# Optimization experiments

Measured on AMD Instinct MI355X. Metric: run time of the kernel, lower is better.

The kernel has to match this reference:

```python
import jax, jax.numpy as jnp
import numpy as np

# config[4]: SparseConv3d(32, 64, k=3, stride=2, pad=1) on a (21,800,704) voxel grid, nnz=220939
IN_DIMS = (21, 800, 704)   # (x, y, z) spatial extents
KSIZE   = (3, 3, 3)
STRIDE  = (2, 2, 2)
PAD     = (1, 1, 1)
CIN, COUT = 32, 64
NNZ = 220939
OUT_DIMS = tuple((IN_DIMS[d] + 2 * PAD[d] - KSIZE[d]) // STRIDE[d] + 1 for d in range(3))  # (11,400,352)


def setup_inputs() -> dict:
    key = jax.random.key(0)
    k1, k2, k3 = jax.random.split(key, 3)
    features = jax.random.normal(k1, (NNZ, CIN), dtype=jnp.float32)
    coords = jnp.stack(
        [jax.random.randint(jax.random.fold_in(k2, d), (NNZ,), 0, IN_DIMS[d]) for d in range(3)],
        axis=1,
    ).astype(jnp.int32)
    # spconv weight layout: one [Cin, Cout] GEMM per kernel offset (27 offsets)
    weight = jax.random.normal(k3, (KSIZE[0] * KSIZE[1] * KSIZE[2], CIN, COUT), dtype=jnp.float32) * 0.05
    return {"features": features, "coords": coords, "weight": weight}


def reference(features, coords, weight):
    # Rulebook gather-GEMM-scatter, vectorized over points; static loop over 27 offsets.
    # out[o] += W[k] @ in[i] where i = o*stride - pad + k, i.e. o = (coord_i + pad - k)/stride.
    n_out = OUT_DIMS[0] * OUT_DIMS[1] * OUT_DIMS[2]
    stride = jnp.array(STRIDE, jnp.int32)
    pad = jnp.array(PAD, jnp.int32)
    odims = jnp.array(OUT_DIMS, jnp.int32)
    out = jnp.zeros((n_out + 1, COUT), features.dtype)  # last row = dump slot for invalid
    kidx = 0
    for kx in range(KSIZE[0]):
        for ky in range(KSIZE[1]):
            for kz in range(KSIZE[2]):
                off = jnp.array([kx, ky, kz], jnp.int32)
                o = coords + pad - off                      # [N,3]
                oq = o // stride
                valid = jnp.all((o >= 0) & (o % stride == 0) & (oq < odims), axis=1)
                flat = (oq[:, 0] * OUT_DIMS[1] + oq[:, 1]) * OUT_DIMS[2] + oq[:, 2]
                flat = jnp.where(valid, flat, n_out)
                contrib = features @ weight[kidx]           # [N, Cout] per-offset GEMM
                out = out.at[flat].add(contrib)             # scatter-accumulate
                kidx += 1
    # Densified sparse-conv output (inactive output sites are exactly zero)
    return out[:-1].reshape(OUT_DIMS + (COUT,))
```

## Files before the change

### kernel.cpp

```cpp
#include <hip/hip_runtime.h>


#define CIN  32
#define COUT 64
#define OXD  11
#define OYD  400
#define OZD  352

constexpr int CHUNKS = 96;

typedef float v2f __attribute__((ext_vector_type(2)));

__global__ __launch_bounds__(256) void zero_out_k(float4* __restrict__ out4,
                                                  int n4, int* __restrict__ gcnt) {
    const int i = blockIdx.x * 256 + threadIdx.x;
    if (i < n4) out4[i] = make_float4(0.f, 0.f, 0.f, 0.f);
    if (i < 27) gcnt[i] = 0;
}

__global__ __launch_bounds__(256) void build_pairs(
    const int* __restrict__ coords, int2* __restrict__ arena,
    int* __restrict__ gcnt, int nnz)
{
    __shared__ int lcnt[27];
    __shared__ int lbase[27];
    const int t = threadIdx.x;
    if (t < 27) lcnt[t] = 0;
    __syncthreads();

    const int n = blockIdx.x * 256 + t;
    int ncomb = 0;
    int ck[8], cls[8], csite[8];
    if (n < nnz) {
        const int cx = coords[3 * n + 0];
        const int cy = coords[3 * n + 1];
        const int cz = coords[3 * n + 2];
        int kxl[2], oxl[2], nx;
        int kyl[2], oyl[2], ny;
        int kzl[2], ozl[2], nz;
        {
            const int c1 = cx + 1;
            if (c1 & 1) { kxl[0] = 1; oxl[0] = c1 >> 1; nx = 1; }
            else { kxl[0] = 2; oxl[0] = (c1 - 2) >> 1; nx = 1;
                   if ((c1 >> 1) < OXD) { kxl[1] = 0; oxl[1] = c1 >> 1; nx = 2; } }
        }
        {
            const int c1 = cy + 1;
            if (c1 & 1) { kyl[0] = 1; oyl[0] = c1 >> 1; ny = 1; }
            else { kyl[0] = 2; oyl[0] = (c1 - 2) >> 1; ny = 1;
                   if ((c1 >> 1) < OYD) { kyl[1] = 0; oyl[1] = c1 >> 1; ny = 2; } }
        }
        {
            const int c1 = cz + 1;
            if (c1 & 1) { kzl[0] = 1; ozl[0] = c1 >> 1; nz = 1; }
            else { kzl[0] = 2; ozl[0] = (c1 - 2) >> 1; nz = 1;
                   if ((c1 >> 1) < OZD) { kzl[1] = 0; ozl[1] = c1 >> 1; nz = 2; } }
        }
        for (int ix = 0; ix < nx; ++ix)
            for (int iy = 0; iy < ny; ++iy)
                for (int iz = 0; iz < nz; ++iz) {
                    const int k = kxl[ix] * 9 + kyl[iy] * 3 + kzl[iz];
                    const int site = (oxl[ix] * OYD + oyl[iy]) * OZD + ozl[iz];
                    ck[ncomb] = k;
                    csite[ncomb] = site;
                    cls[ncomb] = atomicAdd(&lcnt[k], 1);
                    ++ncomb;
                }
    }
    __syncthreads();
    if (t < 27) lbase[t] = atomicAdd(&gcnt[t], lcnt[t]);
    __syncthreads();
    for (int c = 0; c < ncomb; ++c) {
        const int k = ck[c];
        arena[(size_t)k * nnz + lbase[k] + cls[c]] = make_int2(n, csite[c]);
    }
}

__global__ __launch_bounds__(256) void spconv_scatter(
    const float* __restrict__ feat,
    const float* __restrict__ weight,
    const int2*  __restrict__ arena,
    const int*   __restrict__ gcnt,
    float*       __restrict__ out,
    int nnz)
{
    __shared__ float lds[4][8][64][4];

    const int lane = threadIdx.x & 63;
    const int wid  = threadIdx.x >> 6;
    const int k     = blockIdx.x % 27;
    const int chunk = blockIdx.x / 27;
    const int cnt = gcnt[k];
    if (cnt == 0) return;

    v2f w2[16];
    const float* __restrict__ Wk = weight + (size_t)k * CIN * COUT;
    #pragma unroll
    for (int i = 0; i < 16; ++i) {
        w2[i][0] = Wk[(2 * i + 0) * COUT + lane];
        w2[i][1] = Wk[(2 * i + 1) * COUT + lane];
    }

    const int NW = CHUNKS * 4;
    const int widk = chunk * 4 + wid;
    const int C = (cnt + NW - 1) / NW;
    const int start = widk * C;
    const int end   = min(start + C, cnt);
    const int2* __restrict__ ak = arena + (size_t)k * nnz;
    float* __restrict__ outl = out + lane;

    for (int i0 = start; i0 < end; i0 += 64) {
        const int take = min(64, end - i0);
        const int idx = min(i0 + lane, end - 1);
        const int2 pr = ak[idx];

        const float4* __restrict__ fr4 = (const float4*)(feat + (size_t)pr.x * CIN);
        float4 r[8];
        #pragma unroll
        for (int b = 0; b < 8; ++b) r[b] = fr4[b];
        #pragma unroll
        for (int b = 0; b < 8; ++b) *(float4*)&lds[wid][b][lane][0] = r[b];
        asm volatile("s_waitcnt lgkmcnt(0)" ::: "memory");

        for (int j = 0; j < take; ++j) {
            v2f a0 = {0.f, 0.f}, a1 = {0.f, 0.f};
            #pragma unroll
            for (int b = 0; b < 8; ++b) {
                const float4 f = *(const float4*)&lds[wid][b][j][0];
                v2f f01 = {f.x, f.y};
                v2f f23 = {f.z, f.w};
#if __has_builtin(__builtin_elementwise_fma)
                a0 = __builtin_elementwise_fma(f01, w2[2 * b + 0], a0);
                a1 = __builtin_elementwise_fma(f23, w2[2 * b + 1], a1);
#else
                a0[0] = fmaf(f01[0], w2[2 * b + 0][0], a0[0]);
                a0[1] = fmaf(f01[1], w2[2 * b + 0][1], a0[1]);
                a1[0] = fmaf(f23[0], w2[2 * b + 1][0], a1[0]);
                a1[1] = fmaf(f23[1], w2[2 * b + 1][1], a1[1]);
#endif
            }
            const int st = __builtin_amdgcn_readlane(pr.y, j);
            const float acc = (a0[0] + a0[1]) + (a1[0] + a1[1]);
            atomicAdd(outl + (size_t)st * COUT, acc);
        }
    }
}

extern "C" void kernel_launch(void* const* d_in, const int* in_sizes, int n_in,
                              void* d_out, int out_size, void* d_ws, size_t ws_size,
                              hipStream_t stream) {
    const float* feat   = (const float*)d_in[0];
    const int*   coords = (const int*)d_in[1];
    const float* weight = (const float*)d_in[2];
    float*       out    = (float*)d_out;
    const int nnz = in_sizes[0] / CIN;

    int2* arena = (int2*)d_ws;
    int*  gcnt  = (int*)(arena + (size_t)27 * nnz);

    const int n4 = out_size / 4;
    zero_out_k<<<(n4 + 255) / 256, 256, 0, stream>>>((float4*)out, n4, gcnt);
    build_pairs<<<(nnz + 255) / 256, 256, 0, stream>>>(coords, arena, gcnt, nnz);
    spconv_scatter<<<27 * CHUNKS, 256, 0, stream>>>(feat, weight, arena, gcnt, out, nnz);
}
```

Measured before the change: 570.4 us.

## Bucket pairs by output tile and accumulate in LDS, removing global zero-fill

Rebuilds the rulebook as per-output-tile buckets of 128 sites, each with a fixed capacity and a global overflow list. One block per bucket sorts its pairs by kernel offset, accumulates contributions with LDS atomics into a 128x64 tile, then writes the whole tile out. This removes the separate global zero pass and replaces global float atomics with coalesced stores. In exchange, features are read directly from global memory per pair, per-thread transposed weights are reloaded whenever the offset changes, and the whole output must be covered by buckets. An overflow path handles buckets that exceed capacity, but anything beyond the overflow cap is silently dropped.

```diff
diff --git a/kernel.cpp b/kernel.cpp
--- a/kernel.cpp
+++ b/kernel.cpp
@@ -1,148 +1,212 @@
 #include <hip/hip_runtime.h>
 
 
-#define CIN  32
-#define COUT 64
-#define OXD  11
-#define OYD  400
-#define OZD  352
-
-constexpr int CHUNKS = 96;
+#define CIN    32
+#define COUT   64
+#define OXD    11
+#define OYD    400
+#define OZD    352
+#define NOUT   (OXD * OYD * OZD)
+#define BSITES 128
+#define NBUCK  (NOUT / BSITES)
+#define CAP    256
+#define OVCAP  32768
+#define NWT    (27 * COUT * CIN)
 
 typedef float v2f __attribute__((ext_vector_type(2)));
 
-__global__ __launch_bounds__(256) void zero_out_k(float4* __restrict__ out4,
-                                                  int n4, int* __restrict__ gcnt) {
+__global__ __launch_bounds__(256) void prep(const float* __restrict__ w,
+                                            float* __restrict__ wt,
+                                            int* __restrict__ gcnt,
+                                            int* __restrict__ ovcnt) {
     const int i = blockIdx.x * 256 + threadIdx.x;
-    if (i < n4) out4[i] = make_float4(0.f, 0.f, 0.f, 0.f);
-    if (i < 27) gcnt[i] = 0;
+    if (i < NWT) {
+        const int k  = i >> 11;
+        const int rm = i & 2047;
+        const int co = rm >> 5;
+        const int ci = rm & 31;
+        wt[i] = w[k * (CIN * COUT) + ci * COUT + co];
+    }
+    if (i < NBUCK) gcnt[i] = 0;
+    if (i == NBUCK) *ovcnt = 0;
 }
 
 __global__ __launch_bounds__(256) void build_pairs(
-    const int* __restrict__ coords, int2* __restrict__ arena,
-    int* __restrict__ gcnt, int nnz)
-{
-    __shared__ int lcnt[27];
-    __shared__ int lbase[27];
-    const int t = threadIdx.x;
-    if (t < 27) lcnt[t] = 0;
-    __syncthreads();
-
-    const int n = blockIdx.x * 256 + t;
-    int ncomb = 0;
-    int ck[8], cls[8], csite[8];
-    if (n < nnz) {
-        const int cx = coords[3 * n + 0];
-        const int cy = coords[3 * n + 1];
-        const int cz = coords[3 * n + 2];
-        int kxl[2], oxl[2], nx;
-        int kyl[2], oyl[2], ny;
-        int kzl[2], ozl[2], nz;
-        {
-            const int c1 = cx + 1;
-            if (c1 & 1) { kxl[0] = 1; oxl[0] = c1 >> 1; nx = 1; }
-            else { kxl[0] = 2; oxl[0] = (c1 - 2) >> 1; nx = 1;
-                   if ((c1 >> 1) < OXD) { kxl[1] = 0; oxl[1] = c1 >> 1; nx = 2; } }
-        }
-        {
-            const int c1 = cy + 1;
-            if (c1 & 1) { kyl[0] = 1; oyl[0] = c1 >> 1; ny = 1; }
-            else { kyl[0] = 2; oyl[0] = (c1 - 2) >> 1; ny = 1;
-                   if ((c1 >> 1) < OYD) { kyl[1] = 0; oyl[1] = c1 >> 1; ny = 2; } }
-        }
-        {
-            const int c1 = cz + 1;
-            if (c1 & 1) { kzl[0] = 1; ozl[0] = c1 >> 1; nz = 1; }
-            else { kzl[0] = 2; ozl[0] = (c1 - 2) >> 1; nz = 1;
-                   if ((c1 >> 1) < OZD) { kzl[1] = 0; ozl[1] = c1 >> 1; nz = 2; } }
-        }
-        for (int ix = 0; ix < nx; ++ix)
-            for (int iy = 0; iy < ny; ++iy)
-                for (int iz = 0; iz < nz; ++iz) {
-                    const int k = kxl[ix] * 9 + kyl[iy] * 3 + kzl[iz];
-                    const int site = (oxl[ix] * OYD + oyl[iy]) * OZD + ozl[iz];
-                    ck[ncomb] = k;
-                    csite[ncomb] = site;
-                    cls[ncomb] = atomicAdd(&lcnt[k], 1);
-                    ++ncomb;
-                }
-    }
-    __syncthreads();
-    if (t < 27) lbase[t] = atomicAdd(&gcnt[t], lcnt[t]);
-    __syncthreads();
-    for (int c = 0; c < ncomb; ++c) {
-        const int k = ck[c];
-        arena[(size_t)k * nnz + lbase[k] + cls[c]] = make_int2(n, csite[c]);
-    }
-}
-
-__global__ __launch_bounds__(256) void spconv_scatter(
-    const float* __restrict__ feat,
-    const float* __restrict__ weight,
-    const int2*  __restrict__ arena,
-    const int*   __restrict__ gcnt,
-    float*       __restrict__ out,
+    const int* __restrict__ coords,
+    int* __restrict__ arena,
+    int* __restrict__ gcnt,
+    int* __restrict__ ovcnt,
+    int2* __restrict__ ovlist,
     int nnz)
 {
-    __shared__ float lds[4][8][64][4];
-
+    const int n = blockIdx.x * 256 + threadIdx.x;
+    if (n >= nnz) return;
+
+    const int cx = coords[3 * n + 0];
+    const int cy = coords[3 * n + 1];
+    const int cz = coords[3 * n + 2];
+
+    int kxl[2], oxl[2], nx;
+    int kyl[2], oyl[2], ny;
+    int kzl[2], ozl[2], nz;
+    {
+        const int c1 = cx + 1;
+        if (c1 & 1) { kxl[0] = 1; oxl[0] = c1 >> 1; nx = 1; }
+        else { kxl[0] = 2; oxl[0] = (c1 - 2) >> 1; nx = 1;
+               if ((c1 >> 1) < OXD) { kxl[1] = 0; oxl[1] = c1 >> 1; nx = 2; } }
+    }
+    {
+        const int c1 = cy + 1;
+        if (c1 & 1) { kyl[0] = 1; oyl[0] = c1 >> 1; ny = 1; }
+        else { kyl[0] = 2; oyl[0] = (c1 - 2) >> 1; ny = 1;
+               if ((c1 >> 1) < OYD) { kyl[1] = 0; oyl[1] = c1 >> 1; ny = 2; } }
+    }
+    {
+        const int c1 = cz + 1;
+        if (c1 & 1) { kzl[0] = 1; ozl[0] = c1 >> 1; nz = 1; }
+        else { kzl[0] = 2; ozl[0] = (c1 - 2) >> 1; nz = 1;
+               if ((c1 >> 1) < OZD) { kzl[1] = 0; ozl[1] = c1 >> 1; nz = 2; } }
+    }
+
+    for (int ix = 0; ix < nx; ++ix)
+        for (int iy = 0; iy < ny; ++iy)
+            for (int iz = 0; iz < nz; ++iz) {
+                const int k    = kxl[ix] * 9 + kyl[iy] * 3 + kzl[iz];
+                const int site = (oxl[ix] * OYD + oyl[iy]) * OZD + ozl[iz];
+                const int bkt  = site >> 7;
+                const int loc  = site & (BSITES - 1);
+                const int slot = atomicAdd(&gcnt[bkt], 1);
+                if (slot < CAP) {
+                    arena[(size_t)bkt * CAP + slot] = (n << 12) | (k << 7) | loc;
+                } else {
+                    const int o = atomicAdd(ovcnt, 1);
+                    if (o < OVCAP) ovlist[o] = make_int2(site, (n << 5) | k);
+                }
+            }
+}
+
+__global__ __launch_bounds__(256, 4) void spconv_scatter(
+    const float* __restrict__ feat,
+    const float* __restrict__ wt,
+    const int*   __restrict__ arena,
+    const int*   __restrict__ gcnt,
+    float*       __restrict__ out)
+{
+    __shared__ float tile[BSITES][COUT];
+    __shared__ int   sorted[CAP];
+    __shared__ int   khist[27];
+    __shared__ int   kbase[27];
+
+    const int t    = threadIdx.x;
+    const int lane = t & 63;
+    const int wid  = t >> 6;
+    const int b    = blockIdx.x;
+    const int cnt  = min(gcnt[b], CAP);
+
+    if (t < 27) khist[t] = 0;
+    __syncthreads();
+
+    int myp = 0, myk = 0;
+    if (t < cnt) {
+        myp = arena[(size_t)b * CAP + t];
+        myk = (myp >> 7) & 31;
+        atomicAdd(&khist[myk], 1);
+    }
+    float4* t4 = (float4*)&tile[0][0];
+    #pragma unroll
+    for (int r = 0; r < 8; ++r) t4[t + r * 256] = make_float4(0.f, 0.f, 0.f, 0.f);
+    __syncthreads();
+
+    if (wid == 0) {
+        const int h = (lane < 27) ? khist[lane] : 0;
+        int v = h;
+        #pragma unroll
+        for (int off = 1; off < 32; off <<= 1) {
+            const int u = __shfl_up(v, off);
+            if (lane >= off) v += u;
+        }
+        if (lane < 27) kbase[lane] = v - h;
+    }
+    __syncthreads();
+    if (t < cnt) {
+        const int pos = atomicAdd(&kbase[myk], 1);
+        sorted[pos] = myp;
+    }
+    __syncthreads();
+
+    const int c  = (cnt + 3) >> 2;
+    const int jb = min(wid * c, cnt);
+    const int je = min(jb + c, cnt);
+    float4 wv[8];
+    int curk = -1;
+    for (int j = jb; j < je; ++j) {
+        const int pk  = __builtin_amdgcn_readfirstlane(sorted[j]);
+        const int k   = (pk >> 7) & 31;
+        const int loc = pk & (BSITES - 1);
+        const int pt  = pk >> 12;
+        if (k != curk) {
+            curk = k;
+            const float4* __restrict__ wp =
+                (const float4*)(wt + ((size_t)k * COUT + lane) * CIN);
+            #pragma unroll
+            for (int bb = 0; bb < 8; ++bb) wv[bb] = wp[bb];
+        }
+        const float4* __restrict__ fp = (const float4*)(feat + (size_t)pt * CIN);
+        v2f a0 = {0.f, 0.f}, a1 = {0.f, 0.f};
+        #pragma unroll
+        for (int bb = 0; bb < 8; ++bb) {
+            const float4 f = fp[bb];
+            const float4 wb = wv[bb];
+            v2f f01 = {f.x, f.y}, f23 = {f.z, f.w};
+            v2f w01 = {wb.x, wb.y}, w23 = {wb.z, wb.w};
+#if __has_builtin(__builtin_elementwise_fma)
+            a0 = __builtin_elementwise_fma(f01, w01, a0);
+            a1 = __builtin_elementwise_fma(f23, w23, a1);
+#else
+            a0[0] = fmaf(f01[0], w01[0], a0[0]);
+            a0[1] = fmaf(f01[1], w01[1], a0[1]);
+            a1[0] = fmaf(f23[0], w23[0], a1[0]);
+            a1[1] = fmaf(f23[1], w23[1], a1[1]);
+#endif
+        }
+        atomicAdd(&tile[loc][lane], (a0[0] + a0[1]) + (a1[0] + a1[1]));
+    }
+    __syncthreads();
+
+    float4* __restrict__ o4 = (float4*)(out + (size_t)b * (BSITES * COUT));
+    #pragma unroll
+    for (int r = 0; r < 8; ++r) o4[t + r * 256] = t4[t + r * 256];
+}
+
+__global__ __launch_bounds__(256) void fixup_overflow(
+    const float* __restrict__ feat,
+    const float* __restrict__ wt,
+    const int2*  __restrict__ ovlist,
+    const int*   __restrict__ ovcnt,
+    float*       __restrict__ out)
+{
     const int lane = threadIdx.x & 63;
-    const int wid  = threadIdx.x >> 6;
-    const int k     = blockIdx.x % 27;
-    const int chunk = blockIdx.x / 27;
-    const int cnt = gcnt[k];
-    if (cnt == 0) return;
-
-    v2f w2[16];
-    const float* __restrict__ Wk = weight + (size_t)k * CIN * COUT;
-    #pragma unroll
-    for (int i = 0; i < 16; ++i) {
-        w2[i][0] = Wk[(2 * i + 0) * COUT + lane];
-        w2[i][1] = Wk[(2 * i + 1) * COUT + lane];
-    }
-
-    const int NW = CHUNKS * 4;
-    const int widk = chunk * 4 + wid;
-    const int C = (cnt + NW - 1) / NW;
-    const int start = widk * C;
-    const int end   = min(start + C, cnt);
-    const int2* __restrict__ ak = arena + (size_t)k * nnz;
-    float* __restrict__ outl = out + lane;
-
-    for (int i0 = start; i0 < end; i0 += 64) {
-        const int take = min(64, end - i0);
-        const int idx = min(i0 + lane, end - 1);
-        const int2 pr = ak[idx];
-
-        const float4* __restrict__ fr4 = (const float4*)(feat + (size_t)pr.x * CIN);
-        float4 r[8];
+    const int gw   = blockIdx.x * 4 + (threadIdx.x >> 6);
+    const int n    = min(*ovcnt, OVCAP);
+    for (int e = gw; e < n; e += 128 * 4) {
+        const int2 r   = ovlist[e];
+        const int site = r.x;
+        const int pt   = r.y >> 5;
+        const int k    = r.y & 31;
+        const float4* __restrict__ wp =
+            (const float4*)(wt + ((size_t)k * COUT + lane) * CIN);
+        const float4* __restrict__ fp = (const float4*)(feat + (size_t)pt * CIN);
+        float acc = 0.f;
         #pragma unroll
-        for (int b = 0; b < 8; ++b) r[b] = fr4[b];
-        #pragma unroll
-        for (int b = 0; b < 8; ++b) *(float4*)&lds[wid][b][lane][0] = r[b];
-        asm volatile("s_waitcnt lgkmcnt(0)" ::: "memory");
-
-        for (int j = 0; j < take; ++j) {
-            v2f a0 = {0.f, 0.f}, a1 = {0.f, 0.f};
-            #pragma unroll
-            for (int b = 0; b < 8; ++b) {
-                const float4 f = *(const float4*)&lds[wid][b][j][0];
-                v2f f01 = {f.x, f.y};
-                v2f f23 = {f.z, f.w};
-#if __has_builtin(__builtin_elementwise_fma)
-                a0 = __builtin_elementwise_fma(f01, w2[2 * b + 0], a0);
-                a1 = __builtin_elementwise_fma(f23, w2[2 * b + 1], a1);
-#else
-                a0[0] = fmaf(f01[0], w2[2 * b + 0][0], a0[0]);
-                a0[1] = fmaf(f01[1], w2[2 * b + 0][1], a0[1]);
-                a1[0] = fmaf(f23[0], w2[2 * b + 1][0], a1[0]);
-                a1[1] = fmaf(f23[1], w2[2 * b + 1][1], a1[1]);
-#endif
-            }
-            const int st = __builtin_amdgcn_readlane(pr.y, j);
-            const float acc = (a0[0] + a0[1]) + (a1[0] + a1[1]);
-            atomicAdd(outl + (size_t)st * COUT, acc);
-        }
+        for (int bb = 0; bb < 8; ++bb) {
+            const float4 f = fp[bb];
+            const float4 w = wp[bb];
+            acc = fmaf(f.x, w.x, acc);
+            acc = fmaf(f.y, w.y, acc);
+            acc = fmaf(f.z, w.z, acc);
+            acc = fmaf(f.w, w.w, acc);
+        }
+        atomicAdd(out + (size_t)site * COUT + lane, acc);
     }
 }
 
@@ -155,11 +219,15 @@
     float*       out    = (float*)d_out;
     const int nnz = in_sizes[0] / CIN;
 
-    int2* arena = (int2*)d_ws;
-    int*  gcnt  = (int*)(arena + (size_t)27 * nnz);
-
-    const int n4 = out_size / 4;
-    zero_out_k<<<(n4 + 255) / 256, 256, 0, stream>>>((float4*)out, n4, gcnt);
-    build_pairs<<<(nnz + 255) / 256, 256, 0, stream>>>(coords, arena, gcnt, nnz);
-    spconv_scatter<<<27 * CHUNKS, 256, 0, stream>>>(feat, weight, arena, gcnt, out, nnz);
-}
+    float* WT     = (float*)d_ws;
+    int*   gcnt   = (int*)(WT + NWT);
+    int*   ovcnt  = gcnt + NBUCK;
+    int2*  ovlist = (int2*)(ovcnt + 2);
+    int*   arena  = (int*)(ovlist + OVCAP);
+
+    prep<<<(NWT + 255) / 256, 256, 0, stream>>>(weight, WT, gcnt, ovcnt);
+    build_pairs<<<(nnz + 255) / 256, 256, 0, stream>>>(coords, arena, gcnt,
+                                                       ovcnt, ovlist, nnz);
+    spconv_scatter<<<NBUCK, 256, 0, stream>>>(feat, WT, arena, gcnt, out);
+    fixup_overflow<<<128, 256, 0, stream>>>(feat, WT, ovlist, ovcnt, out);
+}
```

New measurement: 675.8 us. 18.5% more time.
